# Kernel tuning notes

Measured on AMD Instinct MI355X. Metric: run time of the kernel, lower is better.

Reference implementation:

```python
import jax, jax.numpy as jnp
import numpy as np

N_NODES = 100000
N_EDGES = 640000
HIDDEN = 128


def setup_inputs() -> dict:
    key = jax.random.key(0)
    k_h, k_e, k_w1, k_b1, k_w2, k_b2 = jax.random.split(key, 6)
    h = jax.random.normal(k_h, (N_NODES, HIDDEN), dtype=jnp.float32)
    edge_index = jax.random.randint(k_e, (2, N_EDGES), 0, N_NODES, dtype=jnp.int64)
    # nn.Linear default init: U(-1/sqrt(fan_in), 1/sqrt(fan_in))
    lim1 = 1.0 / np.sqrt(2 * HIDDEN)
    W1 = jax.random.uniform(k_w1, (2 * HIDDEN, HIDDEN), jnp.float32, -lim1, lim1)
    b1 = jax.random.uniform(k_b1, (HIDDEN,), jnp.float32, -lim1, lim1)
    lim2 = 1.0 / np.sqrt(HIDDEN)
    W2 = jax.random.uniform(k_w2, (HIDDEN, 1), jnp.float32, -lim2, lim2)
    b2 = jax.random.uniform(k_b2, (1,), jnp.float32, -lim2, lim2)
    return {"h": h, "edge_index": edge_index, "W1": W1, "b1": b1, "W2": W2, "b2": b2}


def reference(h, edge_index, W1, b1, W2, b2):
    src, dst = edge_index[0], edge_index[1]
    # cat([h[src], h[dst]]) @ W1 == h[src] @ W1[:H] + h[dst] @ W1[H:]
    W1s, W1d = W1[:HIDDEN], W1[HIDDEN:]
    x = h[src] @ W1s + h[dst] @ W1d + b1          # [E, H]
    x = jax.nn.relu(x)
    score = x @ W2 + b2                            # [E, 1]
    return score.squeeze(-1)                       # [E]
```

## Files before the change

### kernel.cpp

```cpp
#include <hip/hip_runtime.h>

#define HIDDEN 128

typedef _Float16 f16x8 __attribute__((ext_vector_type(8)));
typedef _Float16 f16x4 __attribute__((ext_vector_type(4)));
typedef _Float16 f16x2 __attribute__((ext_vector_type(2)));
typedef __fp16   fp16v2 __attribute__((ext_vector_type(2)));
typedef float f32x4 __attribute__((ext_vector_type(4)));

__global__ __launch_bounds__(64) void prep_w(const float* __restrict__ W1,
                                             _Float16* __restrict__ Wpk) {
  const int blk = blockIdx.x;
  const int jt = blk >> 2;
  const int kt = blk & 3;
  const int lane = threadIdx.x;
  const int col = jt * 16 + (lane & 15);
  const int kbase = kt * 32 + (lane >> 4) * 8;
  f16x8 v;
#pragma unroll
  for (int j = 0; j < 8; ++j) {
    const int k = kbase + j;
    const float w = (col < HIDDEN) ? W1[k * HIDDEN + col]
                                   : W1[(HIDDEN + k) * HIDDEN + (col - HIDDEN)];
    v[j] = (_Float16)w;
  }
  *reinterpret_cast<f16x8*>(Wpk + ((size_t)blk * 64 + lane) * 8) = v;
}

__global__ __launch_bounds__(256, 3) void gemm_mfma_v8(
    const float* __restrict__ h, const _Float16* __restrict__ Wpk,
    const float* __restrict__ b1, _Float16* __restrict__ Af,
    _Float16* __restrict__ Bf, int n_nodes, int ntiles) {
  __shared__ __align__(16) char out_lds[16 * 528];

  const int tid = threadIdx.x;
  const int lane = tid & 63;
  const int wave = tid >> 6;
  const int nl = lane & 15;
  const int kgrp = lane >> 4;
  const int jt0 = wave * 4;

  const f16x8* wp = reinterpret_cast<const f16x8*>(Wpk);
  f16x8 wfrag[4][4];
#pragma unroll
  for (int j4 = 0; j4 < 4; ++j4)
#pragma unroll
    for (int kt = 0; kt < 4; ++kt)
      wfrag[j4][kt] = wp[((jt0 + j4) * 4 + kt) * 64 + lane];

  f32x4 binit[4];
#pragma unroll
  for (int j4 = 0; j4 < 4; ++j4) {
    const int jt = jt0 + j4;
    if (jt < 8) {
      binit[j4] = *reinterpret_cast<const f32x4*>(b1 + jt * 16 + kgrp * 4);
    } else {
      binit[j4][0] = 0.f; binit[j4][1] = 0.f; binit[j4][2] = 0.f; binit[j4][3] = 0.f;
    }
  }

  float4 buf[8];
  f16x8 hfrag[4];

  auto LOAD = [&](int tile) {
    int node = tile * 16 + nl;
    if (node >= n_nodes) node = 0;
    const float4* hp = reinterpret_cast<const float4*>(h) +
                       (size_t)node * 32 + kgrp * 2;
#pragma unroll
    for (int kt = 0; kt < 4; ++kt) {
      buf[kt * 2]     = hp[kt * 8];
      buf[kt * 2 + 1] = hp[kt * 8 + 1];
    }
  };

  auto CVT = [&]() {
#pragma unroll
    for (int kt = 0; kt < 4; ++kt) {
      const float4 v0 = buf[kt * 2];
      const float4 v1 = buf[kt * 2 + 1];
      const fp16v2 p0 = __builtin_amdgcn_cvt_pkrtz(v0.x, v0.y);
      const fp16v2 p1 = __builtin_amdgcn_cvt_pkrtz(v0.z, v0.w);
      const fp16v2 p2 = __builtin_amdgcn_cvt_pkrtz(v1.x, v1.y);
      const fp16v2 p3 = __builtin_amdgcn_cvt_pkrtz(v1.z, v1.w);
      hfrag[kt][0] = (_Float16)p0[0]; hfrag[kt][1] = (_Float16)p0[1];
      hfrag[kt][2] = (_Float16)p1[0]; hfrag[kt][3] = (_Float16)p1[1];
      hfrag[kt][4] = (_Float16)p2[0]; hfrag[kt][5] = (_Float16)p2[1];
      hfrag[kt][6] = (_Float16)p3[0]; hfrag[kt][7] = (_Float16)p3[1];
    }
  };

  auto COMPUTE_DSWRITE = [&]() {
    f32x4 acc[4];
#pragma unroll
    for (int j4 = 0; j4 < 4; ++j4) acc[j4] = binit[j4];
#pragma unroll
    for (int kt = 0; kt < 4; ++kt)
#pragma unroll
      for (int j4 = 0; j4 < 4; ++j4)
        acc[j4] = __builtin_amdgcn_mfma_f32_16x16x32_f16(
            wfrag[j4][kt], hfrag[kt], acc[j4], 0, 0, 0);
#pragma unroll
    for (int j4 = 0; j4 < 4; ++j4) {
      const int jt = jt0 + j4;
      const int byte = nl * 528 + ((jt & 7) * 16 + kgrp * 4) * 2 +
                       ((jt >= 8) ? 256 : 0);
      f16x4 v;
      v[0] = (_Float16)acc[j4][0];
      v[1] = (_Float16)acc[j4][1];
      v[2] = (_Float16)acc[j4][2];
      v[3] = (_Float16)acc[j4][3];
      *reinterpret_cast<f16x4*>(out_lds + byte) = v;
    }
  };

  const int cn = tid >> 4;
  const int seg = tid & 15;
  auto COPYOUT = [&](int tile) {
    const int node = tile * 16 + cn;
    if (node < n_nodes) {
      const f16x8 a = *reinterpret_cast<const f16x8*>(out_lds + cn * 528 + seg * 16);
      const f16x8 b = *reinterpret_cast<const f16x8*>(out_lds + cn * 528 + 256 + seg * 16);
      *reinterpret_cast<f16x8*>(Af + (size_t)node * HIDDEN + seg * 8) = a;
      *reinterpret_cast<f16x8*>(Bf + (size_t)node * HIDDEN + seg * 8) = b;
    }
  };

  const int stride = gridDim.x;
  int tile = blockIdx.x;
  if (tile >= ntiles) return;

  LOAD(tile);
  CVT();
  int next = tile + stride;
  if (next < ntiles) LOAD(next);

  while (true) {
    COMPUTE_DSWRITE();
    if (next < ntiles) CVT();
    __syncthreads();
    COPYOUT(tile);
    if (next >= ntiles) break;
    const int next2 = next + stride;
    if (next2 < ntiles) LOAD(next2);
    __syncthreads();
    tile = next;
    next = next2;
  }
}

__global__ __launch_bounds__(256) void edge_score_v4(
    const int* __restrict__ ei, const _Float16* __restrict__ Af,
    const _Float16* __restrict__ Bf, const float* __restrict__ W2,
    const float* __restrict__ b2, float* __restrict__ out, int n_edges) {
  const int wid = (int)((blockIdx.x * 256 + threadIdx.x) >> 6);
  const int lane = threadIdx.x & 63;
  const int e0 = wid * 16;
  if (e0 >= n_edges) return;

  int srcs[16], dsts[16];
#pragma unroll
  for (int k = 0; k < 16; ++k) {
    srcs[k] = ei[e0 + k];
    dsts[k] = ei[n_edges + e0 + k];
  }

  const char* Afc = (const char*)Af;
  const char* Bfc = (const char*)Bf;
  const unsigned int loff = (unsigned int)(lane << 2);

  f16x2 av[16], bv[16];
#pragma unroll
  for (int k = 0; k < 16; ++k) {
    const unsigned int off = ((unsigned int)srcs[k] << 8) + loff;
    av[k] = *reinterpret_cast<const f16x2*>(Afc + off);
  }
#pragma unroll
  for (int k = 0; k < 16; ++k) {
    const unsigned int off = ((unsigned int)dsts[k] << 8) + loff;
    bv[k] = *reinterpret_cast<const f16x2*>(Bfc + off);
  }

  const float2 w2v = reinterpret_cast<const float2*>(W2)[lane];
  const fp16v2 w2h = __builtin_amdgcn_cvt_pkrtz(w2v.x, w2v.y);
  const _Float16 h0 = (_Float16)0.f;

  float p[16];
#pragma unroll
  for (int k = 0; k < 16; ++k) {
    f16x2 s = av[k] + bv[k];
    s[0] = s[0] > h0 ? s[0] : h0;
    s[1] = s[1] > h0 ? s[1] : h0;
    p[k] = __builtin_amdgcn_fdot2(__builtin_bit_cast(fp16v2, s), w2h, 0.f, false);
  }

  auto mrg = [&](float a, float b, int off) {
    const float as = a + __shfl_xor(a, off, 64);
    const float bs = b + __shfl_xor(b, off, 64);
    return (lane & off) ? bs : as;
  };
  float q[8];
#pragma unroll
  for (int i = 0; i < 8; ++i) q[i] = mrg(p[2 * i], p[2 * i + 1], 1);
  float r[4];
#pragma unroll
  for (int i = 0; i < 4; ++i) r[i] = mrg(q[2 * i], q[2 * i + 1], 2);
  float s2[2];
#pragma unroll
  for (int i = 0; i < 2; ++i) s2[i] = mrg(r[2 * i], r[2 * i + 1], 4);
  float t = mrg(s2[0], s2[1], 8);
  t += __shfl_xor(t, 16, 64);
  t += __shfl_xor(t, 32, 64);

  if (lane < 16 && e0 + lane < n_edges) out[e0 + lane] = t + b2[0];
}

__global__ __launch_bounds__(256) void fused_fallback(
    const float* __restrict__ h, const int* __restrict__ ei,
    const float* __restrict__ W1, const float* __restrict__ b1,
    const float* __restrict__ W2, const float* __restrict__ b2,
    float* __restrict__ out, int n_edges) {
  const int e = (int)((blockIdx.x * 256 + threadIdx.x) >> 6);
  const int lane = threadIdx.x & 63;
  if (e >= n_edges) return;
  const int src = ei[e], dst = ei[n_edges + e];
  const float* hs = h + (size_t)src * HIDDEN;
  const float* hd = h + (size_t)dst * HIDDEN;
  float acc0 = b1[lane], acc1 = b1[lane + 64];
  for (int k = 0; k < HIDDEN; ++k) {
    const float s = hs[k], d = hd[k];
    acc0 = fmaf(s, W1[k * HIDDEN + lane], acc0);
    acc0 = fmaf(d, W1[(k + HIDDEN) * HIDDEN + lane], acc0);
    acc1 = fmaf(s, W1[k * HIDDEN + lane + 64], acc1);
    acc1 = fmaf(d, W1[(k + HIDDEN) * HIDDEN + lane + 64], acc1);
  }
  acc0 = acc0 > 0.f ? acc0 : 0.f;
  acc1 = acc1 > 0.f ? acc1 : 0.f;
  float p = fmaf(acc0, W2[lane], acc1 * W2[lane + 64]);
#pragma unroll
  for (int off = 32; off >= 1; off >>= 1) p += __shfl_down(p, off, 64);
  if (lane == 0) out[e] = p + b2[0];
}

extern "C" void kernel_launch(void* const* d_in, const int* in_sizes, int n_in,
                              void* d_out, int out_size, void* d_ws, size_t ws_size,
                              hipStream_t stream) {
  const float* h  = (const float*)d_in[0];
  const int*   ei = (const int*)d_in[1];
  const float* W1 = (const float*)d_in[2];
  const float* b1 = (const float*)d_in[3];
  const float* W2 = (const float*)d_in[4];
  const float* b2 = (const float*)d_in[5];
  float* out = (float*)d_out;

  const int n_nodes = in_sizes[0] / HIDDEN;
  const int n_edges = in_sizes[1] / 2;

  const size_t wpk_halfs  = 64 * 64 * 8;
  const size_t proj_halfs = (size_t)n_nodes * HIDDEN;
  const size_t need = (wpk_halfs + 2 * proj_halfs) * sizeof(_Float16);

  if (ws_size >= need) {
    _Float16* Wpk = (_Float16*)d_ws;
    _Float16* A   = Wpk + wpk_halfs;
    _Float16* B   = A + proj_halfs;

    prep_w<<<64, 64, 0, stream>>>(W1, Wpk);

    const int ntiles = (n_nodes + 15) / 16;
    const int gblocks = ntiles < 1280 ? ntiles : 1280;
    gemm_mfma_v8<<<gblocks, 256, 0, stream>>>(h, Wpk, b1, A, B, n_nodes, ntiles);

    const int nwaves = (n_edges + 15) / 16;
    const int eblocks = (nwaves + 3) / 4;
    edge_score_v4<<<eblocks, 256, 0, stream>>>(ei, A, B, W2, b2, out, n_edges);
  } else {
    const int eblocks = (n_edges + 3) / 4;
    fused_fallback<<<eblocks, 256, 0, stream>>>(h, ei, W1, b1, W2, b2, out, n_edges);
  }
}
```

Measured before the change: 88.65 us.

## Replace persistent grid-stride GEMM loop with fixed four-tile blocks

```diff
diff --git a/kernel.cpp b/kernel.cpp
--- a/kernel.cpp
+++ b/kernel.cpp
@@ -27,11 +27,11 @@
   *reinterpret_cast<f16x8*>(Wpk + ((size_t)blk * 64 + lane) * 8) = v;
 }
 
-__global__ __launch_bounds__(256, 3) void gemm_mfma_v8(
+__global__ __launch_bounds__(256) void gemm_mfma_v9(
     const float* __restrict__ h, const _Float16* __restrict__ Wpk,
     const float* __restrict__ b1, _Float16* __restrict__ Af,
     _Float16* __restrict__ Bf, int n_nodes, int ntiles) {
-  __shared__ __align__(16) char out_lds[16 * 528];
+  __shared__ __align__(16) char out_lds[4 * 16 * 528];
 
   const int tid = threadIdx.x;
   const int lane = tid & 63;
@@ -39,6 +39,8 @@
   const int nl = lane & 15;
   const int kgrp = lane >> 4;
   const int jt0 = wave * 4;
+  const int t0 = blockIdx.x * 4;
+  if (t0 >= ntiles) return;
 
   const f16x8* wp = reinterpret_cast<const f16x8*>(Wpk);
   f16x8 wfrag[4][4];
@@ -59,10 +61,10 @@
     }
   }
 
-  float4 buf[8];
+  float4 buf0[8], buf1[8];
   f16x8 hfrag[4];
 
-  auto LOAD = [&](int tile) {
+  auto LOAD = [&](float4* buf, int tile) {
     int node = tile * 16 + nl;
     if (node >= n_nodes) node = 0;
     const float4* hp = reinterpret_cast<const float4*>(h) +
@@ -74,7 +76,7 @@
     }
   };
 
-  auto CVT = [&]() {
+  auto CVT = [&](const float4* buf) {
 #pragma unroll
     for (int kt = 0; kt < 4; ++kt) {
       const float4 v0 = buf[kt * 2];
@@ -90,7 +92,7 @@
     }
   };
 
-  auto COMPUTE_DSWRITE = [&]() {
+  auto COMPUTE_DSWRITE = [&](int i) {
     f32x4 acc[4];
 #pragma unroll
     for (int j4 = 0; j4 < 4; ++j4) acc[j4] = binit[j4];
@@ -103,8 +105,8 @@
 #pragma unroll
     for (int j4 = 0; j4 < 4; ++j4) {
       const int jt = jt0 + j4;
-      const int byte = nl * 528 + ((jt & 7) * 16 + kgrp * 4) * 2 +
-                       ((jt >= 8) ? 256 : 0);
+      const int byte = i * 8448 + nl * 528 +
+                       ((jt & 7) * 16 + kgrp * 4) * 2 + ((jt >= 8) ? 256 : 0);
       f16x4 v;
       v[0] = (_Float16)acc[j4][0];
       v[1] = (_Float16)acc[j4][1];
@@ -114,38 +116,28 @@
     }
   };
 
+  LOAD(buf0, t0);
+  LOAD(buf1, t0 + 1);
+  CVT(buf0); LOAD(buf0, t0 + 2); COMPUTE_DSWRITE(0);
+  CVT(buf1); LOAD(buf1, t0 + 3); COMPUTE_DSWRITE(1);
+  CVT(buf0);                     COMPUTE_DSWRITE(2);
+  CVT(buf1);                     COMPUTE_DSWRITE(3);
+
+  __syncthreads();
+
   const int cn = tid >> 4;
   const int seg = tid & 15;
-  auto COPYOUT = [&](int tile) {
-    const int node = tile * 16 + cn;
+#pragma unroll
+  for (int i = 0; i < 4; ++i) {
+    const int node = (t0 + i) * 16 + cn;
     if (node < n_nodes) {
-      const f16x8 a = *reinterpret_cast<const f16x8*>(out_lds + cn * 528 + seg * 16);
-      const f16x8 b = *reinterpret_cast<const f16x8*>(out_lds + cn * 528 + 256 + seg * 16);
+      const f16x8 a = *reinterpret_cast<const f16x8*>(
+          out_lds + i * 8448 + cn * 528 + seg * 16);
+      const f16x8 b = *reinterpret_cast<const f16x8*>(
+          out_lds + i * 8448 + cn * 528 + 256 + seg * 16);
       *reinterpret_cast<f16x8*>(Af + (size_t)node * HIDDEN + seg * 8) = a;
       *reinterpret_cast<f16x8*>(Bf + (size_t)node * HIDDEN + seg * 8) = b;
     }
-  };
-
-  const int stride = gridDim.x;
-  int tile = blockIdx.x;
-  if (tile >= ntiles) return;
-
-  LOAD(tile);
-  CVT();
-  int next = tile + stride;
-  if (next < ntiles) LOAD(next);
-
-  while (true) {
-    COMPUTE_DSWRITE();
-    if (next < ntiles) CVT();
-    __syncthreads();
-    COPYOUT(tile);
-    if (next >= ntiles) break;
-    const int next2 = next + stride;
-    if (next2 < ntiles) LOAD(next2);
-    __syncthreads();
-    tile = next;
-    next = next2;
   }
 }
 
@@ -268,8 +260,8 @@
     prep_w<<<64, 64, 0, stream>>>(W1, Wpk);
 
     const int ntiles = (n_nodes + 15) / 16;
-    const int gblocks = ntiles < 1280 ? ntiles : 1280;
-    gemm_mfma_v8<<<gblocks, 256, 0, stream>>>(h, Wpk, b1, A, B, n_nodes, ntiles);
+    const int gblocks = (ntiles + 3) / 4;
+    gemm_mfma_v9<<<gblocks, 256, 0, stream>>>(h, Wpk, b1, A, B, n_nodes, ntiles);
 
     const int nwaves = (n_edges + 15) / 16;
     const int eblocks = (nwaves + 3) / 4;
```

After: 86.99 us. No clear change (-1.9%).
